# Kernel tuning notes

Measured on AMD Instinct MI355X. Metric: run time of the kernel, lower is better.

Reference implementation:

```python
import jax, jax.numpy as jnp
import numpy as np

N_HEAD = 16
WINDOW = 128
CAUSAL = False


def setup_inputs() -> dict:
    key = jax.random.key(0)
    ks = jax.random.split(key, 5)
    B, T, D = 1, 4096, 1024
    x = jax.random.normal(ks[0], (B, T, D), dtype=jnp.float32)
    w_in = jax.random.normal(ks[1], (3 * D, D), dtype=jnp.float32) * 0.02
    b_in = jax.random.normal(ks[2], (3 * D,), dtype=jnp.float32) * 0.02
    w_out = jax.random.normal(ks[3], (D, D), dtype=jnp.float32) * 0.02
    b_out = jax.random.normal(ks[4], (D,), dtype=jnp.float32) * 0.02
    return {"x": x, "w_in": w_in, "b_in": b_in, "w_out": w_out, "b_out": b_out}


def _window_attention(x, w_in, b_in, w_out, b_out):
    B, T, D = x.shape
    H = N_HEAD
    hd = D // H
    scale = 1.0 / jnp.sqrt(jnp.float32(hd))

    # fused in-projection, as in torch nn.MultiheadAttention (y = x @ W^T + b)
    qkv = jnp.einsum('btd,ed->bte', x, w_in) + b_in  # (B, T, 3D)
    q, k, v = jnp.split(qkv, 3, axis=-1)
    # (B, H, T, hd)
    q = q.reshape(B, T, H, hd).transpose(0, 2, 1, 3)
    k = k.reshape(B, T, H, hd).transpose(0, 2, 1, 3)
    v = v.reshape(B, T, H, hd).transpose(0, 2, 1, 3)

    scores = jnp.einsum('bhqd,bhkd->bhqk', q, k) * scale  # (B, H, T, T)

    idx = jnp.arange(T)
    diff = idx[:, None] - idx[None, :]
    if CAUSAL:
        allowed = (diff >= 0) & (diff <= WINDOW)
    else:
        allowed = jnp.abs(diff) <= WINDOW
    NEG = jnp.float32(-1e30)
    scores = jnp.where(allowed[None, None, :, :], scores, NEG)

    attn = jax.nn.softmax(scores, axis=-1)
    ctx = jnp.einsum('bhqk,bhkd->bhqd', attn, v)  # (B, H, T, hd)
    ctx = ctx.transpose(0, 2, 1, 3).reshape(B, T, D)
    out = jnp.einsum('btd,ed->bte', ctx, w_out) + b_out
    return x + out  # residual, as in the module


def reference(x, w_in, b_in, w_out, b_out):
    return _window_attention(x, w_in, b_in, w_out, b_out)
```

## Files before the change

kernel.cpp:

```cpp
#include <hip/hip_runtime.h>

#define T_SEQ 4096
#define DMODEL 1024
#define NHEAD 16
#define HDIM 64
#define WIN 128

typedef __attribute__((ext_vector_type(8))) short bf16x8;
typedef __attribute__((ext_vector_type(4))) float f32x4;
typedef __attribute__((ext_vector_type(4))) unsigned short u16x4;

__device__ __forceinline__ unsigned short f2bf(float f) {
  unsigned int u = __builtin_bit_cast(unsigned int, f);
  return (unsigned short)((u + 0x7fffu + ((u >> 16) & 1u)) >> 16);
}

__device__ __forceinline__ void gload_lds16(const unsigned short* g,
                                            unsigned short* l) {
  __builtin_amdgcn_global_load_lds(
      (const __attribute__((address_space(1))) void*)g,
      (__attribute__((address_space(3))) void*)l, 16, 0, 0);
}

__global__ void convert_all(const float* __restrict__ x,
                            const float* __restrict__ w_in,
                            const float* __restrict__ w_out,
                            unsigned short* __restrict__ x_bf,
                            unsigned short* __restrict__ w_in_bf,
                            unsigned short* __restrict__ w_out_bf) {
  int stride = gridDim.x * blockDim.x;
  int t0 = blockIdx.x * blockDim.x + threadIdx.x;
#define CVT(SRC, DST, N4)                                          \
  for (int i = t0; i < (N4); i += stride) {                        \
    float4 v = reinterpret_cast<const float4*>(SRC)[i];            \
    u16x4 o;                                                       \
    o.x = f2bf(v.x); o.y = f2bf(v.y); o.z = f2bf(v.z); o.w = f2bf(v.w); \
    reinterpret_cast<u16x4*>(DST)[i] = o;                          \
  }
  CVT(x, x_bf, T_SEQ * DMODEL / 4)
  CVT(w_in, w_in_bf, 3 * DMODEL * DMODEL / 4)
  CVT(w_out, w_out_bf, DMODEL * DMODEL / 4)
#undef CVT
}

template <int EPI, int BM, int BN>
__device__ __forceinline__ void gemm_body(
    const unsigned short* __restrict__ A,
    const unsigned short* __restrict__ B,
    const float* __restrict__ bias,
    unsigned short* __restrict__ q_buf,
    unsigned short* __restrict__ k_buf,
    unsigned short* __restrict__ vt_buf,
    const float* __restrict__ x_res,
    float* __restrict__ out) {
  const int K = DMODEL;
  constexpr int NT = DMODEL / 64;
  constexpr int SM = BM / 2, SN = BN / 2;
  constexpr int MR = SM / 16, NR = SN / 16;
  constexpr int AL = BM / 32, BL = BN / 32;
  __shared__ __align__(16) unsigned short As[2 * BM * 64];
  __shared__ __align__(16) unsigned short Bs[2 * BN * 64];

  int tid = threadIdx.x;
  int lane = tid & 63, wave = tid >> 6;
  int wr = wave >> 1, wc = wave & 1;
  int lo = lane & 15, hi = lane >> 4;
  int t0 = blockIdx.y * BM, e0 = blockIdx.x * BN;

  f32x4 acc[MR][NR];
#pragma unroll
  for (int m = 0; m < MR; ++m)
#pragma unroll
    for (int n = 0; n < NR; ++n) acc[m][n] = (f32x4){0.f, 0.f, 0.f, 0.f};

  int c8 = (tid & 7) ^ ((tid >> 3) & 7);
  int srow = tid >> 3;
  const unsigned short* AbaseG = A + (size_t)(t0 + srow) * K + c8 * 8;
  const unsigned short* BbaseG = B + (size_t)(e0 + srow) * K + c8 * 8;
  unsigned short* ldsAu = As + wave * 512;
  unsigned short* ldsBu = Bs + wave * 512;

  auto stage = [&](int tt) {
    int k0 = tt * 64;
    int ab = (tt & 1) * (BM * 64);
    int bb = (tt & 1) * (BN * 64);
#pragma unroll
    for (int l = 0; l < AL; ++l)
      gload_lds16(AbaseG + (size_t)l * 32 * K + k0, ldsAu + l * 2048 + ab);
#pragma unroll
    for (int l = 0; l < BL; ++l)
      gload_lds16(BbaseG + (size_t)l * 32 * K + k0, ldsBu + l * 2048 + bb);
  };

  stage(0);
  asm volatile("s_waitcnt vmcnt(0) lgkmcnt(0)\n\ts_barrier" ::: "memory");

  for (int t = 0; t < NT; ++t) {
    if (t + 1 < NT) stage(t + 1);
    const unsigned short* Ab = As + (t & 1) * (BM * 64);
    const unsigned short* Bb = Bs + (t & 1) * (BN * 64);
    bf16x8 af[MR][2], bfr[NR][2];
#pragma unroll
    for (int m = 0; m < MR; ++m) {
      int row = wr * SM + m * 16 + lo;
#pragma unroll
      for (int ks = 0; ks < 2; ++ks)
        af[m][ks] = *reinterpret_cast<const bf16x8*>(
            &Ab[row * 64 + (((ks << 2) + hi) ^ (row & 7)) * 8]);
    }
#pragma unroll
    for (int n = 0; n < NR; ++n) {
      int row = wc * SN + n * 16 + lo;
#pragma unroll
      for (int ks = 0; ks < 2; ++ks)
        bfr[n][ks] = *reinterpret_cast<const bf16x8*>(
            &Bb[row * 64 + (((ks << 2) + hi) ^ (row & 7)) * 8]);
    }
#pragma unroll
    for (int ks = 0; ks < 2; ++ks)
#pragma unroll
      for (int m = 0; m < MR; ++m)
#pragma unroll
        for (int n = 0; n < NR; ++n)
          acc[m][n] = __builtin_amdgcn_mfma_f32_16x16x32_bf16(af[m][ks], bfr[n][ks],
                                                              acc[m][n], 0, 0, 0);
    asm volatile("s_waitcnt vmcnt(0) lgkmcnt(0)\n\ts_barrier" ::: "memory");
  }

  int t0w = t0 + wr * SM;
  int e0w = e0 + wc * SN;
#pragma unroll
  for (int m = 0; m < MR; ++m) {
#pragma unroll
    for (int n = 0; n < NR; ++n) {
      int e = e0w + n * 16 + lo;
      float bv = bias[e];
      if (EPI == 0) {
        int part = e >> 10;
        int h = (e >> 6) & 15;
        int d = e & 63;
        if (part == 2) {
          int t = t0w + m * 16 + hi * 4;
          u16x4 pk;
          pk.x = f2bf(acc[m][n][0] + bv);
          pk.y = f2bf(acc[m][n][1] + bv);
          pk.z = f2bf(acc[m][n][2] + bv);
          pk.w = f2bf(acc[m][n][3] + bv);
          *reinterpret_cast<u16x4*>(&vt_buf[((size_t)(h * HDIM + d)) * T_SEQ + t]) = pk;
        } else {
          unsigned short* dst = (part == 0) ? q_buf : k_buf;
#pragma unroll
          for (int jj = 0; jj < 4; ++jj) {
            int t = t0w + m * 16 + hi * 4 + jj;
            dst[((size_t)h * T_SEQ + t) * HDIM + d] = f2bf(acc[m][n][jj] + bv);
          }
        }
      } else {
#pragma unroll
        for (int jj = 0; jj < 4; ++jj) {
          int t = t0w + m * 16 + hi * 4 + jj;
          size_t idxo = (size_t)t * DMODEL + e;
          out[idxo] = acc[m][n][jj] + bv + x_res[idxo];
        }
      }
    }
  }
}

__global__ __launch_bounds__(256) void qkv_gemm(
    const unsigned short* __restrict__ A, const unsigned short* __restrict__ B,
    const float* __restrict__ bias, unsigned short* __restrict__ q_buf,
    unsigned short* __restrict__ k_buf, unsigned short* __restrict__ vt_buf) {
  gemm_body<0, 128, 192>(A, B, bias, q_buf, k_buf, vt_buf, nullptr, nullptr);
}

__global__ __launch_bounds__(256) void out_gemm(
    const unsigned short* __restrict__ A, const unsigned short* __restrict__ B,
    const float* __restrict__ bias, const float* __restrict__ x_res,
    float* __restrict__ out) {
  gemm_body<1, 128, 64>(A, B, bias, nullptr, nullptr, nullptr, x_res, out);
}

__global__ __launch_bounds__(256, 1) void win_attn(
    const unsigned short* __restrict__ q_buf,
    const unsigned short* __restrict__ k_buf,
    const unsigned short* __restrict__ vt_buf,
    unsigned short* __restrict__ ctx) {
  __shared__ __align__(16) unsigned short p_lds[4][4][16 * 40];
  int tid = threadIdx.x;
  int wave = tid >> 6;
  int lane = tid & 63;
  int lo = lane & 15, hi = lane >> 4;

  int id = blockIdx.x;
  int sw = (id & 7) * 32 + (id >> 3);
  int job = sw * 4 + wave;
  int h = job >> 6;
  int q0 = (job & 63) * 64;
  const float SC = 0.18033688011112042f;

  bf16x8 aq[4][2];
#pragma unroll
  for (int u = 0; u < 4; ++u) {
    const unsigned short* qrow =
        q_buf + ((size_t)h * T_SEQ + q0 + u * 16 + lo) * HDIM + hi * 8;
    aq[u][0] = *reinterpret_cast<const bf16x8*>(qrow);
    aq[u][1] = *reinterpret_cast<const bf16x8*>(qrow + 32);
  }

  float L[4][4];
  f32x4 o[4][4];
#pragma unroll
  for (int u = 0; u < 4; ++u)
#pragma unroll
    for (int n = 0; n < 4; ++n) {
      o[u][n] = (f32x4){0.f, 0.f, 0.f, 0.f};
      L[u][n] = 0.f;
    }

  int jstart = q0 - WIN; if (jstart < 0) jstart = 0;
  int jend = q0 + 64 + WIN; if (jend > T_SEQ) jend = T_SEQ;

  for (int j0 = jstart; j0 < jend; j0 += 32) {
    bf16x8 kc[2][2];
#pragma unroll
    for (int c = 0; c < 2; ++c) {
      int krow = j0 + c * 16 + lo;
      if (krow > T_SEQ - 1) krow = T_SEQ - 1;
      const unsigned short* kp = k_buf + ((size_t)h * T_SEQ + krow) * HDIM + hi * 8;
      kc[c][0] = *reinterpret_cast<const bf16x8*>(kp);
      kc[c][1] = *reinterpret_cast<const bf16x8*>(kp + 32);
    }
    bf16x8 vc[4];
#pragma unroll
    for (int n = 0; n < 4; ++n)
      vc[n] = *reinterpret_cast<const bf16x8*>(
          vt_buf + ((size_t)(h * HDIM + n * 16 + lo)) * T_SEQ + j0 + hi * 8);
#pragma unroll
    for (int u = 0; u < 4; ++u) {
      f32x4 z[2];
      __builtin_amdgcn_s_setprio(1);
#pragma unroll
      for (int c = 0; c < 2; ++c) {
        z[c] = (f32x4){0.f, 0.f, 0.f, 0.f};
        z[c] = __builtin_amdgcn_mfma_f32_16x16x32_bf16(aq[u][0], kc[c][0], z[c], 0, 0, 0);
        z[c] = __builtin_amdgcn_mfma_f32_16x16x32_bf16(aq[u][1], kc[c][1], z[c], 0, 0, 0);
      }
      __builtin_amdgcn_s_setprio(0);
#pragma unroll
      for (int c = 0; c < 2; ++c) {
        int kj = j0 + c * 16 + lo;
#pragma unroll
        for (int jq = 0; jq < 4; ++jq) {
          int q = q0 + u * 16 + hi * 4 + jq;
          bool ok = (q - kj <= WIN) && (kj - q <= WIN);
          float p = ok ? __builtin_amdgcn_exp2f(z[c][jq] * SC) : 0.f;
          L[u][jq] += p;
          p_lds[wave][u][(hi * 4 + jq) * 40 + c * 16 + lo] = f2bf(p);
        }
      }
    }
    bf16x8 pa[4];
#pragma unroll
    for (int u = 0; u < 4; ++u)
      pa[u] = *reinterpret_cast<const bf16x8*>(&p_lds[wave][u][lo * 40 + hi * 8]);
    __builtin_amdgcn_s_setprio(1);
#pragma unroll
    for (int n = 0; n < 4; ++n)
#pragma unroll
      for (int u = 0; u < 4; ++u)
        o[u][n] = __builtin_amdgcn_mfma_f32_16x16x32_bf16(pa[u], vc[n], o[u][n], 0, 0, 0);
    __builtin_amdgcn_s_setprio(0);
  }
#pragma unroll
  for (int u = 0; u < 4; ++u)
#pragma unroll
    for (int jq = 0; jq < 4; ++jq) {
#pragma unroll
      for (int w = 1; w < 16; w <<= 1) L[u][jq] += __shfl_xor(L[u][jq], w, 64);
    }
#pragma unroll
  for (int u = 0; u < 4; ++u)
#pragma unroll
    for (int jq = 0; jq < 4; ++jq) {
      int t = q0 + u * 16 + hi * 4 + jq;
      float inv = 1.f / L[u][jq];
#pragma unroll
      for (int n = 0; n < 4; ++n)
        ctx[(size_t)t * DMODEL + h * HDIM + n * 16 + lo] = f2bf(o[u][n][jq] * inv);
    }
}

extern "C" void kernel_launch(void* const* d_in, const int* in_sizes, int n_in,
                              void* d_out, int out_size, void* d_ws, size_t ws_size,
                              hipStream_t stream) {
  const float* x = (const float*)d_in[0];
  const float* w_in = (const float*)d_in[1];
  const float* b_in = (const float*)d_in[2];
  const float* w_out = (const float*)d_in[3];
  const float* b_out = (const float*)d_in[4];
  float* out = (float*)d_out;

  char* ws = (char*)d_ws;
  size_t off = 0;
  auto take = [&](size_t bytes) {
    char* p = ws + off;
    off += (bytes + 255) & ~(size_t)255;
    return p;
  };
  unsigned short* x_bf = (unsigned short*)take((size_t)T_SEQ * DMODEL * 2);
  unsigned short* w_in_bf = (unsigned short*)take((size_t)3 * DMODEL * DMODEL * 2);
  unsigned short* w_out_bf = (unsigned short*)take((size_t)DMODEL * DMODEL * 2);
  unsigned short* q_buf = (unsigned short*)take((size_t)T_SEQ * DMODEL * 2);
  unsigned short* k_buf = (unsigned short*)take((size_t)T_SEQ * DMODEL * 2);
  unsigned short* vt_buf = (unsigned short*)take((size_t)T_SEQ * DMODEL * 2 + 8192);
  unsigned short* ctx = (unsigned short*)take((size_t)T_SEQ * DMODEL * 2);

  convert_all<<<2048, 256, 0, stream>>>(x, w_in, w_out, x_bf, w_in_bf, w_out_bf);

  dim3 g1(3 * DMODEL / 192, T_SEQ / 128);
  qkv_gemm<<<g1, 256, 0, stream>>>(x_bf, w_in_bf, b_in, q_buf, k_buf, vt_buf);

  win_attn<<<256, 256, 0, stream>>>(q_buf, k_buf, vt_buf, ctx);

  dim3 g2(DMODEL / 64, T_SEQ / 128);
  out_gemm<<<g2, 256, 0, stream>>>(ctx, w_out_bf, b_out, x, out);
}
```

Before: 87.90 us.

## Replace QKV GEMM with 256x256 eight-wave pipelined kernel using swizzled LDS

Swaps the templated QKV GEMM for a dedicated 512-thread kernel with 256x256 output tiles. Global loads are staged in registers and written into double-buffered, XOR-swizzled LDS across eight interleaved phases per iteration, with wave priority raised around the MFMA bursts. The aim is more data reuse per tile, fewer LDS bank conflicts and better overlap of memory traffic with matrix math. In exchange the grid shrinks to 192 blocks, fewer than the number of CUs. The 128KB LDS footprint also likely limits each CU to one block, which risks leaving the GPU under-filled.

```diff
diff --git a/kernel.cpp b/kernel.cpp
--- a/kernel.cpp
+++ b/kernel.cpp
@@ -43,17 +43,152 @@
 #undef CVT
 }
 
-template <int EPI, int BM, int BN>
-__device__ __forceinline__ void gemm_body(
+__global__ __launch_bounds__(512, 2) void qkv_gemm8(
     const unsigned short* __restrict__ A,
     const unsigned short* __restrict__ B,
     const float* __restrict__ bias,
     unsigned short* __restrict__ q_buf,
     unsigned short* __restrict__ k_buf,
-    unsigned short* __restrict__ vt_buf,
-    const float* __restrict__ x_res,
+    unsigned short* __restrict__ vt_buf) {
+  const int K = DMODEL;
+  __shared__ __align__(16) unsigned short As[2][256 * 64];
+  __shared__ __align__(16) unsigned short Bs[2][256 * 64];
+
+  int tid = threadIdx.x;
+  int lane = tid & 63, wave = tid >> 6;
+  int wr = wave >> 2, wc = wave & 3;
+  int lo = lane & 15, hi = lane >> 4;
+  int t0 = blockIdx.y * 256, e0 = blockIdx.x * 256;
+  int swrow = wave * 16 + lo;
+  int spos7 = swrow & 7;
+
+  f32x4 acc[8][4];
+#pragma unroll
+  for (int m = 0; m < 8; ++m)
+#pragma unroll
+    for (int n = 0; n < 4; ++n) acc[m][n] = (f32x4){0.f, 0.f, 0.f, 0.f};
+
+  bf16x8 uA0, uA1, uB0, uB1, bfr[4];
+
+  auto ldA = [&](int tt, int kh) {
+    const unsigned short* g =
+        A + (size_t)(t0 + swrow) * K + tt * 64 + kh * 32 + hi * 8;
+    uA0 = *reinterpret_cast<const bf16x8*>(g);
+    uA1 = *reinterpret_cast<const bf16x8*>(g + (size_t)128 * K);
+  };
+  auto ldB = [&](int tt, int kh) {
+    const unsigned short* g =
+        B + (size_t)(e0 + swrow) * K + tt * 64 + kh * 32 + hi * 8;
+    uB0 = *reinterpret_cast<const bf16x8*>(g);
+    uB1 = *reinterpret_cast<const bf16x8*>(g + (size_t)128 * K);
+  };
+  auto wrA = [&](int kh, int buf) {
+    int pos = (((kh << 2) | hi) ^ spos7) * 8;
+    *reinterpret_cast<bf16x8*>(&As[buf][swrow * 64 + pos]) = uA0;
+    *reinterpret_cast<bf16x8*>(&As[buf][(swrow + 128) * 64 + pos]) = uA1;
+  };
+  auto wrB = [&](int kh, int buf) {
+    int pos = (((kh << 2) | hi) ^ spos7) * 8;
+    *reinterpret_cast<bf16x8*>(&Bs[buf][swrow * 64 + pos]) = uB0;
+    *reinterpret_cast<bf16x8*>(&Bs[buf][(swrow + 128) * 64 + pos]) = uB1;
+  };
+
+  ldA(0, 0); wrA(0, 0);
+  ldA(0, 1); wrA(1, 0);
+  ldA(1, 0); wrA(0, 1);
+  ldB(0, 0); wrB(0, 0);
+  ldB(0, 1); wrB(1, 0);
+  ldB(1, 0); wrB(0, 1);
+  ldB(1, 1); wrB(1, 1);
+  ldA(1, 1);
+  ldB(2, 0);
+  __syncthreads();
+
+#define LGKM0() asm volatile("s_waitcnt lgkmcnt(0)" ::: "memory")
+#define BARR() asm volatile("s_barrier" ::: "memory")
+#define PHASE(MH, KS, BUF, WRSTMT, LDSTMT)                                  \
+  {                                                                         \
+    bf16x8 af[4];                                                           \
+    _Pragma("unroll") for (int fm = 0; fm < 4; ++fm) {                      \
+      int grow = wr * 128 + MH * 64 + fm * 16 + lo;                         \
+      af[fm] = *reinterpret_cast<const bf16x8*>(                            \
+          &As[BUF][grow * 64 + ((((KS) << 2) | hi) ^ (grow & 7)) * 8]);     \
+    }                                                                       \
+    if ((MH) == 0) {                                                        \
+      _Pragma("unroll") for (int fn = 0; fn < 4; ++fn) {                    \
+        int brow = wc * 64 + fn * 16 + lo;                                  \
+        bfr[fn] = *reinterpret_cast<const bf16x8*>(                         \
+            &Bs[BUF][brow * 64 + ((((KS) << 2) | hi) ^ (brow & 7)) * 8]);   \
+      }                                                                     \
+    }                                                                       \
+    WRSTMT;                                                                 \
+    LDSTMT;                                                                 \
+    LGKM0();                                                                \
+    BARR();                                                                 \
+    __builtin_amdgcn_s_setprio(1);                                          \
+    _Pragma("unroll") for (int fm = 0; fm < 4; ++fm)                        \
+        _Pragma("unroll") for (int fn = 0; fn < 4; ++fn)                    \
+            acc[(MH) * 4 + fm][fn] = __builtin_amdgcn_mfma_f32_16x16x32_bf16( \
+                af[fm], bfr[fn], acc[(MH) * 4 + fm][fn], 0, 0, 0);          \
+    __builtin_amdgcn_s_setprio(0);                                          \
+    BARR();                                                                 \
+  }
+
+#pragma unroll 1
+  for (int i = 0; i < 8; ++i) {
+    int T2 = 2 * i + 2, T3 = 2 * i + 3, T4 = 2 * i + 4;
+    bool g7 = (i < 7), g6 = (i < 6);
+    PHASE(0, 0, 0, { wrA(1, 1); },            { if (g7) ldA(T2, 0); })
+    PHASE(1, 0, 0, { if (g7) wrB(0, 0); },    { if (g7) ldB(T2, 1); })
+    PHASE(0, 1, 0, { if (g7) wrA(0, 0); },    { if (g7) ldA(T2, 1); })
+    PHASE(1, 1, 0, { if (g7) wrB(1, 0); },    { if (g7) ldB(T3, 0); })
+    PHASE(0, 0, 1, { if (g7) wrA(1, 0); },    { if (g7) ldA(T3, 0); })
+    PHASE(1, 0, 1, { if (g7) wrB(0, 1); },    { if (g7) ldB(T3, 1); })
+    PHASE(0, 1, 1, { if (g7) wrA(0, 1); },    { if (g7) ldA(T3, 1); })
+    PHASE(1, 1, 1, { if (g7) wrB(1, 1); },    { if (g6) ldB(T4, 0); })
+    (void)T2; (void)T3; (void)T4;
+  }
+#undef PHASE
+#undef BARR
+#undef LGKM0
+
+  int t0w = t0 + wr * 128;
+  int e0w = e0 + wc * 64;
+#pragma unroll
+  for (int m = 0; m < 8; ++m) {
+#pragma unroll
+    for (int n = 0; n < 4; ++n) {
+      int e = e0w + n * 16 + lo;
+      float bv = bias[e];
+      int part = e >> 10;
+      int h = (e >> 6) & 15;
+      int d = e & 63;
+      if (part == 2) {
+        int t = t0w + m * 16 + hi * 4;
+        u16x4 pk;
+        pk.x = f2bf(acc[m][n][0] + bv);
+        pk.y = f2bf(acc[m][n][1] + bv);
+        pk.z = f2bf(acc[m][n][2] + bv);
+        pk.w = f2bf(acc[m][n][3] + bv);
+        *reinterpret_cast<u16x4*>(&vt_buf[((size_t)(h * HDIM + d)) * T_SEQ + t]) = pk;
+      } else {
+        unsigned short* dst = (part == 0) ? q_buf : k_buf;
+#pragma unroll
+        for (int jj = 0; jj < 4; ++jj) {
+          int t = t0w + m * 16 + hi * 4 + jj;
+          dst[((size_t)h * T_SEQ + t) * HDIM + d] = f2bf(acc[m][n][jj] + bv);
+        }
+      }
+    }
+  }
+}
+
+__global__ __launch_bounds__(256) void out_gemm(
+    const unsigned short* __restrict__ A, const unsigned short* __restrict__ B,
+    const float* __restrict__ bias, const float* __restrict__ x_res,
     float* __restrict__ out) {
   const int K = DMODEL;
+  constexpr int BM = 128, BN = 64;
   constexpr int NT = DMODEL / 64;
   constexpr int SM = BM / 2, SN = BN / 2;
   constexpr int MR = SM / 16, NR = SN / 16;
@@ -135,50 +270,14 @@
     for (int n = 0; n < NR; ++n) {
       int e = e0w + n * 16 + lo;
       float bv = bias[e];
-      if (EPI == 0) {
-        int part = e >> 10;
-        int h = (e >> 6) & 15;
-        int d = e & 63;
-        if (part == 2) {
-          int t = t0w + m * 16 + hi * 4;
-          u16x4 pk;
-          pk.x = f2bf(acc[m][n][0] + bv);
-          pk.y = f2bf(acc[m][n][1] + bv);
-          pk.z = f2bf(acc[m][n][2] + bv);
-          pk.w = f2bf(acc[m][n][3] + bv);
-          *reinterpret_cast<u16x4*>(&vt_buf[((size_t)(h * HDIM + d)) * T_SEQ + t]) = pk;
-        } else {
-          unsigned short* dst = (part == 0) ? q_buf : k_buf;
-#pragma unroll
-          for (int jj = 0; jj < 4; ++jj) {
-            int t = t0w + m * 16 + hi * 4 + jj;
-            dst[((size_t)h * T_SEQ + t) * HDIM + d] = f2bf(acc[m][n][jj] + bv);
-          }
-        }
-      } else {
-#pragma unroll
-        for (int jj = 0; jj < 4; ++jj) {
-          int t = t0w + m * 16 + hi * 4 + jj;
-          size_t idxo = (size_t)t * DMODEL + e;
-          out[idxo] = acc[m][n][jj] + bv + x_res[idxo];
-        }
+#pragma unroll
+      for (int jj = 0; jj < 4; ++jj) {
+        int t = t0w + m * 16 + hi * 4 + jj;
+        size_t idxo = (size_t)t * DMODEL + e;
+        out[idxo] = acc[m][n][jj] + bv + x_res[idxo];
       }
     }
   }
-}
-
-__global__ __launch_bounds__(256) void qkv_gemm(
-    const unsigned short* __restrict__ A, const unsigned short* __restrict__ B,
-    const float* __restrict__ bias, unsigned short* __restrict__ q_buf,
-    unsigned short* __restrict__ k_buf, unsigned short* __restrict__ vt_buf) {
-  gemm_body<0, 128, 192>(A, B, bias, q_buf, k_buf, vt_buf, nullptr, nullptr);
-}
-
-__global__ __launch_bounds__(256) void out_gemm(
-    const unsigned short* __restrict__ A, const unsigned short* __restrict__ B,
-    const float* __restrict__ bias, const float* __restrict__ x_res,
-    float* __restrict__ out) {
-  gemm_body<1, 128, 64>(A, B, bias, nullptr, nullptr, nullptr, x_res, out);
 }
 
 __global__ __launch_bounds__(256, 1) void win_attn(
@@ -318,8 +417,8 @@
 
   convert_all<<<2048, 256, 0, stream>>>(x, w_in, w_out, x_bf, w_in_bf, w_out_bf);
 
-  dim3 g1(3 * DMODEL / 192, T_SEQ / 128);
-  qkv_gemm<<<g1, 256, 0, stream>>>(x_bf, w_in_bf, b_in, q_buf, k_buf, vt_buf);
+  dim3 g1(3 * DMODEL / 256, T_SEQ / 256);
+  qkv_gemm8<<<g1, 512, 0, stream>>>(x_bf, w_in_bf, b_in, q_buf, k_buf, vt_buf);
 
   win_attn<<<256, 256, 0, stream>>>(q_buf, k_buf, vt_buf, ctx);
 
```

After: 100.1 us. 1.14x slower.
